# Optimization experiments

Hardware: AMD Instinct MI355X
Metric: run time of the kernel (lower is better)

The kernel has to match this reference:

```python
import jax, jax.numpy as jnp
import numpy as np

B, S, D, H = 16, 512, 768, 12
DH = D // H


def setup_inputs() -> dict:
    key = jax.random.key(0)
    ks = jax.random.split(key, 12)
    hidden_states = jax.random.normal(ks[0], (B, S, D), dtype=jnp.float32)
    # additive padding mask: 0 for valid, -10000 for padded tail tokens
    lengths = jax.random.randint(ks[1], (B,), S // 2, S + 1)
    pad = (jnp.arange(S)[None, :] >= lengths[:, None]).astype(jnp.float32)
    attention_mask = (pad * -10000.0)[:, None, None, :]  # [B,1,1,S]
    # row-stochastic graph prior over codes
    pr = jax.random.uniform(ks[2], (B, S, S), dtype=jnp.float32)
    prior = pr / jnp.sum(pr, axis=-1, keepdims=True)
    s = 0.02
    params = dict(
        Wq=jax.random.normal(ks[3], (D, D)) * s, bq=jnp.zeros((D,)),
        Wk=jax.random.normal(ks[4], (D, D)) * s, bk=jnp.zeros((D,)),
        Wv=jax.random.normal(ks[5], (D, D)) * s, bv=jnp.zeros((D,)),
        Wg=jax.random.normal(ks[6], (D, 2)) * s, bg=jnp.zeros((2,)),
        Wo=jax.random.normal(ks[7], (D, D)) * s, bo=jnp.zeros((D,)),
        gamma=jnp.ones((D,)), beta=jnp.zeros((D,)),
    )
    return dict(hidden_states=hidden_states, attention_mask=attention_mask,
                prior=prior, **params)


def _layer_norm(x, gamma, beta, eps=1e-5):
    mu = jnp.mean(x, axis=-1, keepdims=True)
    var = jnp.mean(jnp.square(x - mu), axis=-1, keepdims=True)
    return (x - mu) * jax.lax.rsqrt(var + eps) * gamma + beta


def reference(hidden_states, attention_mask, prior,
              Wq, bq, Wk, bk, Wv, bv, Wg, bg, Wo, bo, gamma, beta):
    b, s, d = hidden_states.shape
    # project and split heads: [B,S,H,DH]
    q = (hidden_states @ Wq + bq).reshape(b, s, H, DH)
    k = (hidden_states @ Wk + bk).reshape(b, s, H, DH)
    v = (hidden_states @ Wv + bv).reshape(b, s, H, DH)
    scores = jnp.einsum('bshd,bthd->bhst', q, k) / jnp.sqrt(jnp.float32(DH))
    scores = scores + attention_mask  # broadcast [B,1,1,S]
    probs = jax.nn.softmax(scores, axis=-1)  # [B,H,S,S]
    # gate: avg-pool over valid tokens, softmax(linear/2)
    valid = (attention_mask.squeeze((1, 2)) == 0.0).astype(hidden_states.dtype)  # [B,S]
    denom = jnp.maximum(jnp.sum(valid, axis=1, keepdims=True), 1.0)
    h_pool = jnp.sum(hidden_states * valid[:, :, None], axis=1) / denom  # [B,D]
    gate = jax.nn.softmax((h_pool @ Wg + bg) / 2.0, axis=-1)  # [B,2]
    probs = probs * gate[:, 0, None, None, None] + prior[:, None, :, :] * gate[:, 1, None, None, None]
    ctx = jnp.einsum('bhst,bthd->bshd', probs, v).reshape(b, s, d)
    out = jax.nn.relu(ctx @ Wo + bo)
    out = _layer_norm(out + hidden_states, gamma, beta)
    return out
```

## Files before the change

kernel.cpp:

```cpp
#include <hip/hip_runtime.h>

#define NB_ 16
#define S_ 512
#define D_ 768
#define H_ 12
#define DH_ 64
#define QT_ 64
#define KT_ 128

typedef __attribute__((ext_vector_type(8))) short bf16x8;
typedef __attribute__((ext_vector_type(4))) float f32x4;
typedef unsigned short ushort_t;

__device__ __forceinline__ unsigned short f2bf(float f){
  unsigned int u = __float_as_uint(f);
  u += 0x7fffu + ((u >> 16) & 1u);
  return (unsigned short)(u >> 16);
}
__device__ __forceinline__ float bf2f(unsigned short s){
  return __uint_as_float(((unsigned int)s) << 16);
}
__device__ __forceinline__ unsigned int pack2(float a, float b){
  return (unsigned int)f2bf(a) | ((unsigned int)f2bf(b) << 16);
}
__device__ __forceinline__ void gld16(const ushort_t* g, ushort_t* l){
  __builtin_amdgcn_global_load_lds((const __attribute__((address_space(1))) unsigned int*)g,
                                   (__attribute__((address_space(3))) unsigned int*)l, 16, 0, 0);
}

__global__ __launch_bounds__(256) void k_wtrans(const float* __restrict__ W0, const float* __restrict__ W1,
                                                const float* __restrict__ W2, const float* __restrict__ W3,
                                                ushort_t* __restrict__ dst){
  const float* W = (blockIdx.z == 0) ? W0 : (blockIdx.z == 1) ? W1 : (blockIdx.z == 2) ? W2 : W3;
  ushort_t* o = dst + (size_t)blockIdx.z * D_ * D_;
  __shared__ float t[32][33];
  int j = threadIdx.x & 31, i0 = threadIdx.x >> 5;
  int kb = blockIdx.y * 32, nb = blockIdx.x * 32;
#pragma unroll
  for (int r = 0; r < 4; r++){
    int i = i0 + r * 8;
    t[i][j] = W[(size_t)(kb + i) * D_ + nb + j];
  }
  __syncthreads();
#pragma unroll
  for (int r = 0; r < 4; r++){
    int i = i0 + r * 8;
    o[(size_t)(nb + i) * D_ + kb + j] = f2bf(t[j][i]);
  }
}

__global__ __launch_bounds__(256) void k_bias3(const float* __restrict__ b0, const float* __restrict__ b1,
                                               const float* __restrict__ b2, float* __restrict__ o){
  int i = blockIdx.x * 256 + threadIdx.x;
  if (i < 3 * D_){
    float v = (i < D_) ? b0[i] : (i < 2 * D_) ? b1[i - D_] : b2[i - 2 * D_];
    o[i] = v;
  }
}

__global__ __launch_bounds__(256) void k_prep(const float* __restrict__ hs, const float* __restrict__ mask,
                                              ushort_t* __restrict__ hsb,
                                              float* __restrict__ partial, float* __restrict__ pcnt){
  int chunk = blockIdx.x, b = blockIdx.y, tid = threadIdx.x;
  const float* mrow = mask + b * S_ + chunk * 64;
  const float* base = hs + ((size_t)b * S_ + chunk * 64) * D_;
  ushort_t* obase = hsb + ((size_t)b * S_ + chunk * 64) * D_;
  float a0 = 0.f, a1 = 0.f, a2 = 0.f, cnt = 0.f;
#pragma unroll 2
  for (int s = 0; s < 64; s++){
    const float* r = base + (size_t)s * D_;
    float x0 = r[tid], x1 = r[tid + 256], x2 = r[tid + 512];
    ushort_t* o = obase + (size_t)s * D_;
    o[tid] = f2bf(x0); o[tid + 256] = f2bf(x1); o[tid + 512] = f2bf(x2);
    if (mrow[s] == 0.0f){ a0 += x0; a1 += x1; a2 += x2; cnt += 1.0f; }
  }
  float* o = partial + (size_t)(b * 8 + chunk) * D_;
  o[tid] = a0; o[tid + 256] = a1; o[tid + 512] = a2;
  if (tid == 0) pcnt[b * 8 + chunk] = cnt;
}

__global__ __launch_bounds__(256) void k_pool2(const float* __restrict__ partial, const float* __restrict__ pcnt,
                                               const float* __restrict__ Wg, const float* __restrict__ bg,
                                               float* __restrict__ gate){
  int b = blockIdx.x, tid = threadIdx.x;
  __shared__ float red[256];
  __shared__ float hp[768];
  float a0 = 0.f, a1 = 0.f, a2 = 0.f;
#pragma unroll
  for (int c = 0; c < 8; c++){
    const float* p = partial + (size_t)(b * 8 + c) * D_;
    a0 += p[tid]; a1 += p[tid + 256]; a2 += p[tid + 512];
  }
  float denom = 0.f;
#pragma unroll
  for (int c = 0; c < 8; c++) denom += pcnt[b * 8 + c];
  float inv = 1.0f / fmaxf(denom, 1.0f);
  hp[tid] = a0 * inv; hp[tid + 256] = a1 * inv; hp[tid + 512] = a2 * inv;
  __syncthreads();
  float p0 = 0.f, p1 = 0.f;
  for (int d = tid; d < D_; d += 256){ p0 += hp[d] * Wg[d * 2]; p1 += hp[d] * Wg[d * 2 + 1]; }
  red[tid] = p0; __syncthreads();
  for (int o = 128; o > 0; o >>= 1){ if (tid < o) red[tid] += red[tid + o]; __syncthreads(); }
  float z0 = red[0]; __syncthreads();
  red[tid] = p1; __syncthreads();
  for (int o = 128; o > 0; o >>= 1){ if (tid < o) red[tid] += red[tid + o]; __syncthreads(); }
  float z1 = red[0];
  if (tid == 0){
    z0 = (z0 + bg[0]) * 0.5f; z1 = (z1 + bg[1]) * 0.5f;
    float m = fmaxf(z0, z1);
    float e0 = __expf(z0 - m), e1 = __expf(z1 - m);
    float ssum = e0 + e1;
    gate[b * 2] = e0 / ssum; gate[b * 2 + 1] = e1 / ssum;
  }
}

template<int OUTBF16, int RELU, int RESID, int AFP32, int MAP>
__global__ __launch_bounds__(256) void k_gemm_bt(
    const void* __restrict__ Ap, long sA, int lda,
    const ushort_t* __restrict__ Bm, long sB, int ldb,
    void* __restrict__ Cp, long sC, int ldc,
    const float* __restrict__ bias,
    const float* __restrict__ resid, float alpha, int K)
{
  __shared__ ushort_t As[128 * 64];
  __shared__ ushort_t Bs[128 * 64];
  int z, bm, bn;
  if (MAP == 2){ z = blockIdx.x; bm = blockIdx.y; bn = blockIdx.z; }
  else if (MAP == 1){ z = blockIdx.z; bm = blockIdx.x; bn = blockIdx.y; }
  else { z = blockIdx.z; bm = blockIdx.y; bn = blockIdx.x; }
  const ushort_t* Ab = AFP32 ? nullptr : ((const ushort_t*)Ap + (size_t)z * sA);
  const float*    Af = AFP32 ? ((const float*)Ap + (size_t)z * sA) : nullptr;
  const ushort_t* Bb = Bm + (size_t)z * sB;
  const long coff = (long)z * sC;
  const int tid = threadIdx.x;
  const int m0 = bm * 128, n0 = bn * 128;
  const int wid = tid >> 6, lane = tid & 63;
  const int quad = lane >> 4, l16 = lane & 15;
  const int wm = wid >> 1, wn = wid & 1;
  const int sw = l16 & 7;

  f32x4 acc[4][4];
#pragma unroll
  for (int i = 0; i < 4; i++)
#pragma unroll
    for (int j = 0; j < 4; j++) acc[i][j] = (f32x4){0.f, 0.f, 0.f, 0.f};

  for (int k0 = 0; k0 < K; k0 += 64){
#pragma unroll
    for (int c = 0; c < 4; c++){
      int idx = tid + c * 256;
      int row = idx >> 3, p = idx & 7;
      int cg = p ^ (row & 7);
      if (AFP32){
        const float* src = Af + (size_t)(m0 + row) * lda + k0 + cg * 8;
        float4 f0 = *(const float4*)src;
        float4 f1 = *(const float4*)(src + 4);
        uint4 pk;
        pk.x = pack2(f0.x, f0.y);
        pk.y = pack2(f0.z, f0.w);
        pk.z = pack2(f1.x, f1.y);
        pk.w = pack2(f1.z, f1.w);
        *(uint4*)(&As[idx * 8]) = pk;
      } else {
        gld16(Ab + (size_t)(m0 + row) * lda + k0 + cg * 8, &As[idx * 8]);
      }
    }
#pragma unroll
    for (int c = 0; c < 4; c++){
      int idx = tid + c * 256;
      int row = idx >> 3, p = idx & 7;
      int cg = p ^ (row & 7);
      gld16(Bb + (size_t)(n0 + row) * ldb + k0 + cg * 8, &Bs[idx * 8]);
    }
    __syncthreads();
#pragma unroll
    for (int ks = 0; ks < 2; ks++){
      bf16x8 af[4], bfv[4];
#pragma unroll
      for (int mi = 0; mi < 4; mi++){
        int row = wm * 64 + mi * 16 + l16;
        af[mi] = *(const bf16x8*)(&As[(row * 8 + ((ks * 4 + quad) ^ sw)) * 8]);
      }
#pragma unroll
      for (int ni = 0; ni < 4; ni++){
        int row = wn * 64 + ni * 16 + l16;
        bfv[ni] = *(const bf16x8*)(&Bs[(row * 8 + ((ks * 4 + quad) ^ sw)) * 8]);
      }
#pragma unroll
      for (int mi = 0; mi < 4; mi++)
#pragma unroll
        for (int ni = 0; ni < 4; ni++)
          acc[mi][ni] = __builtin_amdgcn_mfma_f32_16x16x32_bf16(af[mi], bfv[ni], acc[mi][ni], 0, 0, 0);
    }
    __syncthreads();
  }

#pragma unroll
  for (int mi = 0; mi < 4; mi++){
#pragma unroll
    for (int ni = 0; ni < 4; ni++){
      int col = n0 + wn * 64 + ni * 16 + l16;
      float bcol = bias ? bias[col] : 0.0f;
#pragma unroll
      for (int r = 0; r < 4; r++){
        int row = m0 + wm * 64 + mi * 16 + quad * 4 + r;
        float v = acc[mi][ni][r] * alpha + bcol;
        if (RELU) v = fmaxf(v, 0.0f);
        if (RESID) v += resid[(size_t)row * ldc + col];
        long idx = coff + (long)row * ldc + col;
        if (OUTBF16) ((ushort_t*)Cp)[idx] = f2bf(v);
        else         ((float*)Cp)[idx] = v;
      }
    }
  }
}

__global__ __launch_bounds__(256) void k_vtrans(const ushort_t* __restrict__ v, int ldv,
                                                ushort_t* __restrict__ vt){
  __shared__ ushort_t t[64][66];
  int st = blockIdx.x * 64; int z = blockIdx.y;
  int b = z / H_, h = z - b * H_;
  int tid = threadIdx.x;
  const ushort_t* src = v + ((size_t)b * S_ + st) * ldv + h * DH_;
#pragma unroll
  for (int rep = 0; rep < 8; rep++){
    int idx = rep * 256 + tid;
    int i = idx >> 5, u = idx & 31;
    unsigned int val = *(const unsigned int*)(src + (size_t)i * ldv + u * 2);
    *(unsigned int*)(&t[i][u * 2]) = val;
  }
  __syncthreads();
  ushort_t* dst = vt + (size_t)z * DH_ * S_ + st;
#pragma unroll
  for (int rep = 0; rep < 8; rep++){
    int idx = rep * 256 + tid;
    int d = idx >> 5, u2 = idx & 31;
    unsigned int val = (unsigned int)t[u2 * 2][d] | ((unsigned int)t[u2 * 2 + 1][d] << 16);
    *(unsigned int*)(dst + (size_t)d * S_ + u2 * 2) = val;
  }
}

__global__ __launch_bounds__(256) void k_flash(
    const ushort_t* __restrict__ qkv,
    const ushort_t* __restrict__ vt,
    const ushort_t* __restrict__ priorctx,
    const float* __restrict__ mask,
    const float* __restrict__ gate,
    ushort_t* __restrict__ ctx)
{
  __shared__ ushort_t Qs[QT_ * 72];
  __shared__ ushort_t Ks[KT_ * 72];
  __shared__ ushort_t Vs[DH_ * 136];
  __shared__ ushort_t Ps[QT_ * 136];
  __shared__ float rs[QT_];
  const int z = blockIdx.x, b = z / H_, h = z - b * H_;
  const int q0 = blockIdx.y * QT_;
  const int tid = threadIdx.x;
  const int wid = tid >> 6, lane = tid & 63, quad = lane >> 4, l16 = lane & 15;

#pragma unroll
  for (int i = 0; i < 2; i++){
    int c = tid + i * 256;
    int row = c >> 3, off = (c & 7) * 8;
    *(float4*)(&Qs[row * 72 + off]) =
      *(const float4*)(qkv + ((size_t)(b * S_ + q0 + row)) * 2304 + h * DH_ + off);
  }
  if (tid < QT_) rs[tid] = 0.f;

  f32x4 accv[4];
#pragma unroll
  for (int ni = 0; ni < 4; ni++) accv[ni] = (f32x4){0.f, 0.f, 0.f, 0.f};

  for (int t0 = 0; t0 < S_; t0 += KT_){
    if (mask[b * S_ + t0] != 0.0f) break;
#pragma unroll
    for (int i = 0; i < 4; i++){
      int c = tid + i * 256;
      int row = c >> 3, off = (c & 7) * 8;
      *(float4*)(&Ks[row * 72 + off]) =
        *(const float4*)(qkv + ((size_t)(b * S_ + t0 + row)) * 2304 + D_ + h * DH_ + off);
    }
#pragma unroll
    for (int i = 0; i < 4; i++){
      int c = tid + i * 256;
      int row = c >> 4, off = (c & 15) * 8;
      *(float4*)(&Vs[row * 136 + off]) =
        *(const float4*)(vt + (size_t)z * (DH_ * S_) + (size_t)row * S_ + t0 + off);
    }
    __syncthreads();

    f32x4 accs[2][4];
#pragma unroll
    for (int mi = 0; mi < 2; mi++)
#pragma unroll
      for (int ni = 0; ni < 4; ni++) accs[mi][ni] = (f32x4){0.f, 0.f, 0.f, 0.f};
    bf16x8 ak[2][2], bq[4][2];
#pragma unroll
    for (int mi = 0; mi < 2; mi++)
#pragma unroll
      for (int ks = 0; ks < 2; ks++)
        ak[mi][ks] = *(const bf16x8*)(&Ks[(wid * 32 + mi * 16 + l16) * 72 + ks * 32 + quad * 8]);
#pragma unroll
    for (int ni = 0; ni < 4; ni++)
#pragma unroll
      for (int ks = 0; ks < 2; ks++)
        bq[ni][ks] = *(const bf16x8*)(&Qs[(ni * 16 + l16) * 72 + ks * 32 + quad * 8]);
#pragma unroll
    for (int mi = 0; mi < 2; mi++)
#pragma unroll
      for (int ni = 0; ni < 4; ni++){
        accs[mi][ni] = __builtin_amdgcn_mfma_f32_16x16x32_bf16(ak[mi][0], bq[ni][0], accs[mi][ni], 0, 0, 0);
        accs[mi][ni] = __builtin_amdgcn_mfma_f32_16x16x32_bf16(ak[mi][1], bq[ni][1], accs[mi][ni], 0, 0, 0);
      }

    float mv[2][4];
#pragma unroll
    for (int mi = 0; mi < 2; mi++)
#pragma unroll
      for (int r = 0; r < 4; r++)
        mv[mi][r] = mask[b * S_ + t0 + wid * 32 + mi * 16 + quad * 4 + r];
    float rowpart[4] = {0.f, 0.f, 0.f, 0.f};
#pragma unroll
    for (int mi = 0; mi < 2; mi++){
#pragma unroll
      for (int ni = 0; ni < 4; ni++){
        float e0 = __expf(accs[mi][ni][0] * 0.125f + mv[mi][0]);
        float e1 = __expf(accs[mi][ni][1] * 0.125f + mv[mi][1]);
        float e2 = __expf(accs[mi][ni][2] * 0.125f + mv[mi][2]);
        float e3 = __expf(accs[mi][ni][3] * 0.125f + mv[mi][3]);
        rowpart[ni] += (e0 + e1) + (e2 + e3);
        uint2 pk;
        pk.x = pack2(e0, e1);
        pk.y = pack2(e2, e3);
        *(uint2*)(&Ps[(ni * 16 + l16) * 136 + wid * 32 + mi * 16 + quad * 4]) = pk;
      }
    }
#pragma unroll
    for (int ni = 0; ni < 4; ni++){
      rowpart[ni] += __shfl_xor(rowpart[ni], 16);
      rowpart[ni] += __shfl_xor(rowpart[ni], 32);
    }
    if (lane < 16){
#pragma unroll
      for (int ni = 0; ni < 4; ni++) atomicAdd(&rs[ni * 16 + l16], rowpart[ni]);
    }
    __syncthreads();

#pragma unroll
    for (int ks = 0; ks < 4; ks++){
      bf16x8 ap = *(const bf16x8*)(&Ps[(wid * 16 + l16) * 136 + ks * 32 + quad * 8]);
#pragma unroll
      for (int ni = 0; ni < 4; ni++){
        bf16x8 bv8 = *(const bf16x8*)(&Vs[(ni * 16 + l16) * 136 + ks * 32 + quad * 8]);
        accv[ni] = __builtin_amdgcn_mfma_f32_16x16x32_bf16(ap, bv8, accv[ni], 0, 0, 0);
      }
    }
    __syncthreads();
  }

  const float g0 = gate[b * 2], g1 = gate[b * 2 + 1];
#pragma unroll
  for (int ni = 0; ni < 4; ni++){
#pragma unroll
    for (int r = 0; r < 4; r++){
      int q = wid * 16 + quad * 4 + r;
      int dh = ni * 16 + l16;
      float scl = g0 / rs[q];
      size_t idx = ((size_t)(b * S_ + q0 + q)) * D_ + h * DH_ + dh;
      float v = accv[ni][r] * scl + g1 * bf2f(priorctx[idx]);
      ctx[idx] = f2bf(v);
    }
  }
}

__global__ __launch_bounds__(256) void k_ln(float* __restrict__ out, const float* __restrict__ gamma,
                                            const float* __restrict__ beta){
  __shared__ float red[256];
  int row = blockIdx.x, tid = threadIdx.x;
  float* p = out + (size_t)row * D_;
  float x0 = p[tid], x1 = p[tid + 256], x2 = p[tid + 512];
  red[tid] = x0 + x1 + x2; __syncthreads();
  for (int o = 128; o > 0; o >>= 1){ if (tid < o) red[tid] += red[tid + o]; __syncthreads(); }
  float mu = red[0] * (1.0f / 768.0f);
  __syncthreads();
  float d0 = x0 - mu, d1 = x1 - mu, d2 = x2 - mu;
  red[tid] = d0 * d0 + d1 * d1 + d2 * d2; __syncthreads();
  for (int o = 128; o > 0; o >>= 1){ if (tid < o) red[tid] += red[tid + o]; __syncthreads(); }
  float rsv = rsqrtf(red[0] * (1.0f / 768.0f) + 1e-5f);
  p[tid]       = d0 * rsv * gamma[tid]       + beta[tid];
  p[tid + 256] = d1 * rsv * gamma[tid + 256] + beta[tid + 256];
  p[tid + 512] = d2 * rsv * gamma[tid + 512] + beta[tid + 512];
}

extern "C" void kernel_launch(void* const* d_in, const int* in_sizes, int n_in,
                              void* d_out, int out_size, void* d_ws, size_t ws_size,
                              hipStream_t stream){
  const float* hs    = (const float*)d_in[0];
  const float* mask  = (const float*)d_in[1];
  const float* prior = (const float*)d_in[2];
  const float* Wq = (const float*)d_in[3];  const float* bq = (const float*)d_in[4];
  const float* Wk = (const float*)d_in[5];  const float* bk = (const float*)d_in[6];
  const float* Wv = (const float*)d_in[7];  const float* bv = (const float*)d_in[8];
  const float* Wg = (const float*)d_in[9];  const float* bg = (const float*)d_in[10];
  const float* Wo = (const float*)d_in[11]; const float* bo = (const float*)d_in[12];
  const float* gamma = (const float*)d_in[13]; const float* beta = (const float*)d_in[14];
  float* out = (float*)d_out;

  size_t off = 0;
  auto alloc = [&](size_t bytes) -> char* {
    char* p = (char*)d_ws + off;
    off += (bytes + 255) & ~(size_t)255;
    return p;
  };
  const size_t HSD = (size_t)NB_ * S_ * D_;
  ushort_t* hsb     = (ushort_t*)alloc(HSD * 2);
  ushort_t* qkvb    = (ushort_t*)alloc(HSD * 3 * 2);
  ushort_t* vtb     = (ushort_t*)alloc(HSD * 2);
  ushort_t* wt      = (ushort_t*)alloc((size_t)4 * D_ * D_ * 2);
  ushort_t* priorctx= (ushort_t*)alloc(HSD * 2);
  ushort_t* ctx     = (ushort_t*)alloc(HSD * 2);
  float*    bqkv    = (float*)alloc((size_t)3 * D_ * 4);
  float*    gate    = (float*)alloc(256);
  float*    partial = (float*)alloc((size_t)NB_ * 8 * D_ * 4);
  float*    pcnt    = (float*)alloc((size_t)NB_ * 8 * 4);

  k_prep<<<dim3(8, NB_), 256, 0, stream>>>(hs, mask, hsb, partial, pcnt);
  k_wtrans<<<dim3(24, 24, 4), 256, 0, stream>>>(Wq, Wk, Wv, Wo, wt);
  k_bias3<<<dim3(9), 256, 0, stream>>>(bq, bk, bv, bqkv);
  k_pool2<<<dim3(NB_), 256, 0, stream>>>(partial, pcnt, Wg, bg, gate);
  k_gemm_bt<1, 0, 0, 0, 1><<<dim3(64, 18, 1), 256, 0, stream>>>(
      hsb, 0, D_, wt, 0, D_, qkvb, 0, 3 * D_, bqkv, nullptr, 1.0f, D_);
  k_vtrans<<<dim3(S_ / 64, NB_ * H_), 256, 0, stream>>>(qkvb + 2 * D_, 3 * D_, vtb);
  k_gemm_bt<1, 0, 0, 1, 2><<<dim3(16, 4, 6), 256, 0, stream>>>(
      prior, (long)S_ * S_, S_, vtb, (long)H_ * DH_ * S_, S_,
      priorctx, (long)S_ * D_, D_, nullptr, nullptr, 1.0f, S_);
  k_flash<<<dim3(NB_ * H_, S_ / QT_), 256, 0, stream>>>(
      qkvb, vtb, priorctx, mask, gate, ctx);
  k_gemm_bt<0, 1, 1, 0, 1><<<dim3(64, 6, 1), 256, 0, stream>>>(
      ctx, 0, D_, wt + 3 * (size_t)D_ * D_, 0, D_, out, 0, D_, bo, hs, 1.0f, D_);
  k_ln<<<dim3(NB_ * S_), 256, 0, stream>>>(out, gamma, beta);
}
```

Measured before the change: 300.3 us.

## Keep Q in registers and stream K/V into XOR-swizzled LDS directly

Q fragments are now loaded once straight from global memory into registers, and the Q shared-memory tile is removed. K and V tiles are loaded with the gld16 direct global-to-LDS path into unpadded buffers that use an XOR swizzle, replacing the padded layout while still avoiding bank conflicts. The goal is less LDS traffic, less LDS footprint and fewer VGPR round trips in the flash-attention loop. In exchange, the Q loads from global are strided and not coalesced, and the kernel keeps more registers live across the loop.

After: 291.6 us. 2.9% less time.

```diff
diff --git a/kernel.cpp b/kernel.cpp
--- a/kernel.cpp
+++ b/kernel.cpp
@@ -248,9 +248,8 @@
     const float* __restrict__ gate,
     ushort_t* __restrict__ ctx)
 {
-  __shared__ ushort_t Qs[QT_ * 72];
-  __shared__ ushort_t Ks[KT_ * 72];
-  __shared__ ushort_t Vs[DH_ * 136];
+  __shared__ ushort_t Ks[KT_ * 64];
+  __shared__ ushort_t Vs[DH_ * 128];
   __shared__ ushort_t Ps[QT_ * 136];
   __shared__ float rs[QT_];
   const int z = blockIdx.x, b = z / H_, h = z - b * H_;
@@ -258,13 +257,13 @@
   const int tid = threadIdx.x;
   const int wid = tid >> 6, lane = tid & 63, quad = lane >> 4, l16 = lane & 15;
 
-#pragma unroll
-  for (int i = 0; i < 2; i++){
-    int c = tid + i * 256;
-    int row = c >> 3, off = (c & 7) * 8;
-    *(float4*)(&Qs[row * 72 + off]) =
-      *(const float4*)(qkv + ((size_t)(b * S_ + q0 + row)) * 2304 + h * DH_ + off);
-  }
+  bf16x8 bq[4][2];
+#pragma unroll
+  for (int ni = 0; ni < 4; ni++)
+#pragma unroll
+    for (int ks = 0; ks < 2; ks++)
+      bq[ni][ks] = *(const bf16x8*)(qkv + ((size_t)(b * S_ + q0 + ni * 16 + l16)) * 2304
+                                    + h * DH_ + ks * 32 + quad * 8);
   if (tid < QT_) rs[tid] = 0.f;
 
   f32x4 accv[4];
@@ -274,18 +273,18 @@
   for (int t0 = 0; t0 < S_; t0 += KT_){
     if (mask[b * S_ + t0] != 0.0f) break;
 #pragma unroll
-    for (int i = 0; i < 4; i++){
-      int c = tid + i * 256;
-      int row = c >> 3, off = (c & 7) * 8;
-      *(float4*)(&Ks[row * 72 + off]) =
-        *(const float4*)(qkv + ((size_t)(b * S_ + t0 + row)) * 2304 + D_ + h * DH_ + off);
-    }
-#pragma unroll
-    for (int i = 0; i < 4; i++){
-      int c = tid + i * 256;
-      int row = c >> 4, off = (c & 15) * 8;
-      *(float4*)(&Vs[row * 136 + off]) =
-        *(const float4*)(vt + (size_t)z * (DH_ * S_) + (size_t)row * S_ + t0 + off);
+    for (int c = 0; c < 4; c++){
+      int idx = tid + c * 256;
+      int row = idx >> 3, p = idx & 7;
+      int cg = p ^ (row & 7);
+      gld16(qkv + ((size_t)(b * S_ + t0 + row)) * 2304 + D_ + h * DH_ + cg * 8, &Ks[idx * 8]);
+    }
+#pragma unroll
+    for (int c = 0; c < 4; c++){
+      int idx = tid + c * 256;
+      int row = idx >> 4, p = idx & 15;
+      int cg = p ^ (row & 15);
+      gld16(vt + (size_t)z * (DH_ * S_) + (size_t)row * S_ + t0 + cg * 8, &Vs[idx * 8]);
     }
     __syncthreads();
 
@@ -294,24 +293,20 @@
     for (int mi = 0; mi < 2; mi++)
 #pragma unroll
       for (int ni = 0; ni < 4; ni++) accs[mi][ni] = (f32x4){0.f, 0.f, 0.f, 0.f};
-    bf16x8 ak[2][2], bq[4][2];
-#pragma unroll
-    for (int mi = 0; mi < 2; mi++)
-#pragma unroll
-      for (int ks = 0; ks < 2; ks++)
-        ak[mi][ks] = *(const bf16x8*)(&Ks[(wid * 32 + mi * 16 + l16) * 72 + ks * 32 + quad * 8]);
-#pragma unroll
-    for (int ni = 0; ni < 4; ni++)
-#pragma unroll
-      for (int ks = 0; ks < 2; ks++)
-        bq[ni][ks] = *(const bf16x8*)(&Qs[(ni * 16 + l16) * 72 + ks * 32 + quad * 8]);
-#pragma unroll
-    for (int mi = 0; mi < 2; mi++)
-#pragma unroll
-      for (int ni = 0; ni < 4; ni++){
-        accs[mi][ni] = __builtin_amdgcn_mfma_f32_16x16x32_bf16(ak[mi][0], bq[ni][0], accs[mi][ni], 0, 0, 0);
-        accs[mi][ni] = __builtin_amdgcn_mfma_f32_16x16x32_bf16(ak[mi][1], bq[ni][1], accs[mi][ni], 0, 0, 0);
-      }
+#pragma unroll
+    for (int ks = 0; ks < 2; ks++){
+      bf16x8 ak[2];
+#pragma unroll
+      for (int mi = 0; mi < 2; mi++){
+        int row = wid * 32 + mi * 16 + l16;
+        ak[mi] = *(const bf16x8*)(&Ks[(row * 8 + ((ks * 4 + quad) ^ (l16 & 7))) * 8]);
+      }
+#pragma unroll
+      for (int mi = 0; mi < 2; mi++)
+#pragma unroll
+        for (int ni = 0; ni < 4; ni++)
+          accs[mi][ni] = __builtin_amdgcn_mfma_f32_16x16x32_bf16(ak[mi], bq[ni][ks], accs[mi][ni], 0, 0, 0);
+    }
 
     float mv[2][4];
 #pragma unroll
@@ -351,7 +346,7 @@
       bf16x8 ap = *(const bf16x8*)(&Ps[(wid * 16 + l16) * 136 + ks * 32 + quad * 8]);
 #pragma unroll
       for (int ni = 0; ni < 4; ni++){
-        bf16x8 bv8 = *(const bf16x8*)(&Vs[(ni * 16 + l16) * 136 + ks * 32 + quad * 8]);
+        bf16x8 bv8 = *(const bf16x8*)(&Vs[((ni * 16 + l16) * 16 + ((ks * 4 + quad) ^ l16)) * 8]);
         accv[ni] = __builtin_amdgcn_mfma_f32_16x16x32_bf16(ap, bv8, accv[ni], 0, 0, 0);
       }
     }
```
